# Kernel optimization log

Measured on AMD Instinct MI355X. Metric: run time of the kernel, lower is better.

Reference implementation:

```python
import jax, jax.numpy as jnp
import numpy as np

HID = 128
OUT = 5


def _gru_layer(x, kernel, rkernel, bias):
    # Keras GRU v2 semantics, reset_after=True, activation=tanh, recurrent_activation=sigmoid.
    # x: [B, T, F]; kernel: [F, 3H]; rkernel: [H, 3H]; bias: [2, 3H] (input bias, recurrent bias)
    b_in, b_rec = bias[0], bias[1]
    H = rkernel.shape[0]
    xw = jnp.einsum('btf,fh->bth', x, kernel) + b_in  # precompute input projections [B,T,3H]

    def step(h, xw_t):
        ri = h @ rkernel + b_rec                      # [B, 3H]
        xz, xr, xh = jnp.split(xw_t, 3, axis=-1)
        rz, rr, rh = jnp.split(ri, 3, axis=-1)
        z = jax.nn.sigmoid(xz + rz)
        r = jax.nn.sigmoid(xr + rr)
        hh = jnp.tanh(xh + r * rh)
        h_new = z * h + (1.0 - z) * hh
        return h_new, h_new

    h0 = jnp.zeros((x.shape[0], H), dtype=x.dtype)
    _, hs = jax.lax.scan(step, h0, jnp.swapaxes(xw, 0, 1))  # [T, B, H]
    return jnp.swapaxes(hs, 0, 1)                           # [B, T, H]


def setup_inputs() -> dict:
    key = jax.random.key(0)
    ks = jax.random.split(key, 12)
    B, T, F = 64, 2048, 128
    s = 1.0 / np.sqrt(F)
    inp = {"x": jax.random.normal(ks[0], (B, T, F), dtype=jnp.float32)}
    for i in range(3):
        fin = F if i == 0 else HID
        inp[f"k{i}"] = jax.random.normal(ks[1 + 3 * i], (fin, 3 * HID), dtype=jnp.float32) * s
        inp[f"rk{i}"] = jax.random.normal(ks[2 + 3 * i], (HID, 3 * HID), dtype=jnp.float32) * s
        inp[f"b{i}"] = jnp.zeros((2, 3 * HID), dtype=jnp.float32)
    inp["wo"] = jax.random.normal(ks[10], (HID, OUT), dtype=jnp.float32) * s
    inp["bo"] = jnp.zeros((OUT,), dtype=jnp.float32)
    return inp


def reference(x, k0, rk0, b0, k1, rk1, b1, k2, rk2, b2, wo, bo):
    h = _gru_layer(x, k0, rk0, b0)
    h = _gru_layer(h, k1, rk1, b1)
    h = _gru_layer(h, k2, rk2, b2)
    return h @ wo + bo  # [B, T, OUT]
```

## Files before the change

kernel.cpp:

```cpp
#include <hip/hip_runtime.h>
#include <hip/hip_bf16.h>
#include <hip/hip_fp16.h>


#define HID   128
#define H3    384
#define OUTD  5
#define CHK   16

typedef _Float16 f16x2 __attribute__((ext_vector_type(2)));
typedef _Float16 f16x8 __attribute__((ext_vector_type(8)));

__device__ __forceinline__ float fdot2(f16x2 a, f16x2 b, float c) {
#if __has_builtin(__builtin_amdgcn_fdot2)
    return __builtin_amdgcn_fdot2(a, b, c, false);
#else
    return fmaf((float)a.x, (float)b.x, fmaf((float)a.y, (float)b.y, c));
#endif
}

__device__ __forceinline__ float fexp2(float x) {
#if __has_builtin(__builtin_amdgcn_exp2f)
    return __builtin_amdgcn_exp2f(x);
#else
    return exp2f(x);
#endif
}

__device__ __forceinline__ float frcp(float x) {
#if __has_builtin(__builtin_amdgcn_rcpf)
    return __builtin_amdgcn_rcpf(x);
#else
    return 1.f / x;
#endif
}

__device__ __forceinline__ float fsigmoid(float x) {
    return frcp(1.f + fexp2(x * -1.4426950408889634f));
}

__device__ __forceinline__ float ftanh_(float x) {
    return fmaf(-2.f, frcp(1.f + fexp2(x * 2.8853900817779268f)), 1.f);
}

__device__ __forceinline__ void soft_barrier() {
    asm volatile("s_waitcnt lgkmcnt(0)\n\ts_barrier" ::: "memory");
}

__device__ __forceinline__ float quad_sum(float x) {
#if __has_builtin(__builtin_amdgcn_mov_dpp)
    int i1 = __builtin_amdgcn_mov_dpp(__float_as_int(x), 0xB1, 0xF, 0xF, true);
    x += __int_as_float(i1);
    int i2 = __builtin_amdgcn_mov_dpp(__float_as_int(x), 0x4E, 0xF, 0xF, true);
    x += __int_as_float(i2);
#else
    x += __shfl_xor(x, 1);
    x += __shfl_xor(x, 2);
#endif
    return x;
}

__global__ void zero_flags(int* f) {
    if (threadIdx.x < 192) f[threadIdx.x] = 0;
}

__global__ __launch_bounds__(512, 2) void gru_pipe(
    const float* __restrict__ x,
    const float* __restrict__ k0, const float* __restrict__ k1, const float* __restrict__ k2,
    const float* __restrict__ rk0, const float* __restrict__ rk1, const float* __restrict__ rk2,
    const float* __restrict__ b0, const float* __restrict__ b1, const float* __restrict__ b2,
    _Float16* __restrict__ hpl0, _Float16* __restrict__ hpl1, _Float16* __restrict__ hpl2,
    int* flags, int T)
{
    const int blk   = blockIdx.x;
    const int layer = blk >> 6;
    const int b     = blk & 63;
    const int t     = threadIdx.x;
    const int j     = t >> 2;
    const int kh    = t & 3;
    const int k0i   = kh * 32;
    const int NC    = T / CHK;

    const float* Kw = (layer == 0) ? k0  : (layer == 1) ? k1  : k2;
    const float* Rw = (layer == 0) ? rk0 : (layer == 1) ? rk1 : rk2;
    const float* Bs = (layer == 0) ? b0  : (layer == 1) ? b1  : b2;
    const _Float16* hin = (layer == 1) ? hpl0 : hpl1;
    _Float16* hout = (layer == 0) ? hpl0 : (layer == 1) ? hpl1 : hpl2;

    __shared__ __align__(16) _Float16 hb[2][HID];
    __shared__ __align__(16) _Float16 ins[2][CHK][HID];

    f16x2 wzR[16], wrR[16], whR[16], wzK[16], wrK[16], whK[16];
#pragma unroll
    for (int p = 0; p < 16; ++p) {
        const int k = k0i + 2 * p;
        const float* r0p = Rw + (size_t)k * H3;
        const float* r1p = Rw + (size_t)(k + 1) * H3;
        const float* k0p = Kw + (size_t)k * H3;
        const float* k1p = Kw + (size_t)(k + 1) * H3;
        f16x2 a;
        a.x = (_Float16)r0p[j];       a.y = (_Float16)r1p[j];       wzR[p] = a;
        a.x = (_Float16)r0p[j + 128]; a.y = (_Float16)r1p[j + 128]; wrR[p] = a;
        a.x = (_Float16)r0p[j + 256]; a.y = (_Float16)r1p[j + 256]; whR[p] = a;
        a.x = (_Float16)k0p[j];       a.y = (_Float16)k1p[j];       wzK[p] = a;
        a.x = (_Float16)k0p[j + 128]; a.y = (_Float16)k1p[j + 128]; wrK[p] = a;
        a.x = (_Float16)k0p[j + 256]; a.y = (_Float16)k1p[j + 256]; whK[p] = a;
    }
    const float bzK = Bs[j]       + Bs[384 + j];
    const float brK = Bs[128 + j] + Bs[384 + 128 + j];
    const float bhK = Bs[256 + j];
    const float bhR = Bs[384 + 256 + j];

    int* myflag = flags + layer * 64 + b;
    int* sflag  = flags + (layer - 1) * 64 + b;

    const float*    xb  = x    + (size_t)b * T * HID;
    const _Float16* hib = hin  + (size_t)b * T * HID;
    _Float16*       hob = hout + (size_t)b * T * HID;

    f16x2 sreg[2];
    auto stage_load = [&](int cc) {
#pragma unroll
        for (int i = 0; i < 2; ++i) {
            const int d  = t + 512 * i;
            const int rw = d >> 6;
            const int c2 = d & 63;
            const size_t off = (size_t)(cc * CHK + rw) * HID + 2 * c2;
            if (layer == 0) {
                const float2 v = *(const float2*)(xb + off);
                f16x2 o; o.x = (_Float16)v.x; o.y = (_Float16)v.y;
                sreg[i] = o;
            } else {
                sreg[i] = *(const f16x2*)(hib + off);
            }
        }
    };
    auto stage_write = [&](int cc) {
        const int slot = cc & 1;
#pragma unroll
        for (int i = 0; i < 2; ++i) {
            const int d  = t + 512 * i;
            const int rw = d >> 6;
            const int c2 = d & 63;
            *(f16x2*)(&ins[slot][rw][2 * c2]) = sreg[i];
        }
    };

    if (t < HID) { hb[0][t] = (_Float16)0.f; hb[1][t] = (_Float16)0.f; }

    if (layer > 0 && t == 0) {
        while (__hip_atomic_load(sflag, __ATOMIC_ACQUIRE, __HIP_MEMORY_SCOPE_AGENT) < CHK)
            __builtin_amdgcn_s_sleep(4);
    }
    __syncthreads();
    stage_load(0);
    stage_write(0);
    __syncthreads();

    float xz, xr, xh;
    {
        const f16x8* ip = (const f16x8*)(&ins[0][0][k0i]);
        float pz = 0.f, pr = 0.f, ph = 0.f;
#pragma unroll
        for (int i = 0; i < 4; ++i) {
            union { f16x8 v; f16x2 p[4]; } u;
            u.v = ip[i];
#pragma unroll
            for (int q = 0; q < 4; ++q) {
                pz = fdot2(u.p[q], wzK[4 * i + q], pz);
                pr = fdot2(u.p[q], wrK[4 * i + q], pr);
                ph = fdot2(u.p[q], whK[4 * i + q], ph);
            }
        }
        xz = quad_sum(pz) + bzK;
        xr = quad_sum(pr) + brK;
        xh = quad_sum(ph) + bhK;
    }

    float h_old = 0.f;

    for (int c = 0; c < NC; ++c) {
        __syncthreads();
        if (t == 0) {
            if (layer < 2 && c > 0)
                __hip_atomic_store(myflag, c * CHK, __ATOMIC_RELEASE, __HIP_MEMORY_SCOPE_AGENT);
            if (layer > 0 && c + 1 < NC) {
                while (__hip_atomic_load(sflag, __ATOMIC_ACQUIRE, __HIP_MEMORY_SCOPE_AGENT) < (c + 2) * CHK)
                    __builtin_amdgcn_s_sleep(4);
            }
        }
        __syncthreads();
        if (c + 1 < NC) stage_load(c + 1);

#pragma unroll 2
        for (int ts = 0; ts < CHK; ++ts) {
            const int tstep = c * CHK + ts;
            const int rbuf  = ts & 1;

            const f16x8* hp = (const f16x8*)(&hb[rbuf][k0i]);
            float sz = 0.f, sr = 0.f, sh = 0.f;
#pragma unroll
            for (int i = 0; i < 4; ++i) {
                union { f16x8 v; f16x2 p[4]; } u;
                u.v = hp[i];
#pragma unroll
                for (int q = 0; q < 4; ++q) {
                    sz = fdot2(u.p[q], wzR[4 * i + q], sz);
                    sr = fdot2(u.p[q], wrR[4 * i + q], sr);
                    sh = fdot2(u.p[q], whR[4 * i + q], sh);
                }
            }
            sz = quad_sum(sz); sr = quad_sum(sr); sh = quad_sum(sh);

            const float z  = fsigmoid(xz + sz);
            const float r  = fsigmoid(xr + sr);
            const float hh = ftanh_(xh + (sh + bhR) * r);
            const float hn = fmaf(z, h_old - hh, hh);
            h_old = hn;

            if (kh == 0) {
                hb[rbuf ^ 1][j] = (_Float16)hn;
                hob[(size_t)tstep * HID + j] = (_Float16)hn;
            }

            if (ts == 7 && c + 1 < NC) stage_write(c + 1);

            if (tstep + 1 < T) {
                const int tn = tstep + 1;
                const f16x8* ip = (const f16x8*)(&ins[(tn >> 4) & 1][tn & 15][k0i]);
                float pz = 0.f, pr = 0.f, ph = 0.f;
#pragma unroll
                for (int i = 0; i < 4; ++i) {
                    union { f16x8 v; f16x2 p[4]; } u;
                    u.v = ip[i];
#pragma unroll
                    for (int q = 0; q < 4; ++q) {
                        pz = fdot2(u.p[q], wzK[4 * i + q], pz);
                        pr = fdot2(u.p[q], wrK[4 * i + q], pr);
                        ph = fdot2(u.p[q], whK[4 * i + q], ph);
                    }
                }
                xz = quad_sum(pz) + bzK;
                xr = quad_sum(pr) + brK;
                xh = quad_sum(ph) + bhK;
            }

            soft_barrier();
        }
    }

    __syncthreads();
    if (t == 0 && layer < 2)
        __hip_atomic_store(myflag, T, __ATOMIC_RELEASE, __HIP_MEMORY_SCOPE_AGENT);
}

__global__ __launch_bounds__(256) void out_proj(
    const _Float16* __restrict__ Hf,
    const float* __restrict__ wo,
    const float* __restrict__ bo,
    float*       __restrict__ out,
    int R)
{
    const int r = blockIdx.x * 256 + threadIdx.x;
    if (r >= R) return;
    const f16x8* xp = (const f16x8*)(Hf + (size_t)r * HID);

    float a0 = bo[0], a1 = bo[1], a2 = bo[2], a3 = bo[3], a4 = bo[4];
#pragma unroll 4
    for (int c = 0; c < 16; ++c) {
        const f16x8 v = xp[c];
#pragma unroll
        for (int e = 0; e < 8; ++e) {
            const float xv = (float)v[e];
            const float* w = wo + (size_t)(8 * c + e) * OUTD;
            a0 = fmaf(xv, w[0], a0);
            a1 = fmaf(xv, w[1], a1);
            a2 = fmaf(xv, w[2], a2);
            a3 = fmaf(xv, w[3], a3);
            a4 = fmaf(xv, w[4], a4);
        }
    }
    float* op = out + (size_t)r * OUTD;
    op[0] = a0; op[1] = a1; op[2] = a2; op[3] = a3; op[4] = a4;
}

extern "C" void kernel_launch(void* const* d_in, const int* in_sizes, int n_in,
                              void* d_out, int out_size, void* d_ws, size_t ws_size,
                              hipStream_t stream) {
    const float* x   = (const float*)d_in[0];
    const float* k0  = (const float*)d_in[1];
    const float* rk0 = (const float*)d_in[2];
    const float* b0  = (const float*)d_in[3];
    const float* k1  = (const float*)d_in[4];
    const float* rk1 = (const float*)d_in[5];
    const float* b1  = (const float*)d_in[6];
    const float* k2  = (const float*)d_in[7];
    const float* rk2 = (const float*)d_in[8];
    const float* b2  = (const float*)d_in[9];
    const float* wo  = (const float*)d_in[10];
    const float* bo  = (const float*)d_in[11];
    float* out = (float*)d_out;

    const int BT = in_sizes[0] / HID;
    const int B  = 64;
    const int T  = BT / B;

    const size_t plane = (size_t)BT * HID * sizeof(_Float16);
    _Float16* hpl0 = (_Float16*)d_ws;
    _Float16* hpl1 = (_Float16*)((char*)d_ws + plane);
    _Float16* hpl2 = (_Float16*)((char*)d_ws + 2 * plane);
    int*      flags = (int*)((char*)d_ws + 3 * plane);

    zero_flags<<<1, 256, 0, stream>>>(flags);
    gru_pipe  <<<192, 512, 0, stream>>>(x, k0, k1, k2, rk0, rk1, rk2,
                                        b0, b1, b2, hpl0, hpl1, hpl2, flags, T);
    out_proj  <<<(BT + 255) / 256, 256, 0, stream>>>(hpl2, wo, bo, out, BT);
}
```

Baseline: 1.752 ms.

## Warp-specialize GRU block: dedicated waves compute input projection one step ahead

```diff
diff --git a/kernel.cpp b/kernel.cpp
--- a/kernel.cpp
+++ b/kernel.cpp
@@ -60,11 +60,21 @@
     return x;
 }
 
+__device__ __forceinline__ float pair_sum(float x) {
+#if __has_builtin(__builtin_amdgcn_mov_dpp)
+    int i1 = __builtin_amdgcn_mov_dpp(__float_as_int(x), 0xB1, 0xF, 0xF, true);
+    x += __int_as_float(i1);
+#else
+    x += __shfl_xor(x, 1);
+#endif
+    return x;
+}
+
 __global__ void zero_flags(int* f) {
     if (threadIdx.x < 192) f[threadIdx.x] = 0;
 }
 
-__global__ __launch_bounds__(512, 2) void gru_pipe(
+__global__ __launch_bounds__(768, 3) void gru_pipe(
     const float* __restrict__ x,
     const float* __restrict__ k0, const float* __restrict__ k1, const float* __restrict__ k2,
     const float* __restrict__ rk0, const float* __restrict__ rk1, const float* __restrict__ rk2,
@@ -76,9 +86,6 @@
     const int layer = blk >> 6;
     const int b     = blk & 63;
     const int t     = threadIdx.x;
-    const int j     = t >> 2;
-    const int kh    = t & 3;
-    const int k0i   = kh * 32;
     const int NC    = T / CHK;
 
     const float* Kw = (layer == 0) ? k0  : (layer == 1) ? k1  : k2;
@@ -89,27 +96,7 @@
 
     __shared__ __align__(16) _Float16 hb[2][HID];
     __shared__ __align__(16) _Float16 ins[2][CHK][HID];
-
-    f16x2 wzR[16], wrR[16], whR[16], wzK[16], wrK[16], whK[16];
-#pragma unroll
-    for (int p = 0; p < 16; ++p) {
-        const int k = k0i + 2 * p;
-        const float* r0p = Rw + (size_t)k * H3;
-        const float* r1p = Rw + (size_t)(k + 1) * H3;
-        const float* k0p = Kw + (size_t)k * H3;
-        const float* k1p = Kw + (size_t)(k + 1) * H3;
-        f16x2 a;
-        a.x = (_Float16)r0p[j];       a.y = (_Float16)r1p[j];       wzR[p] = a;
-        a.x = (_Float16)r0p[j + 128]; a.y = (_Float16)r1p[j + 128]; wrR[p] = a;
-        a.x = (_Float16)r0p[j + 256]; a.y = (_Float16)r1p[j + 256]; whR[p] = a;
-        a.x = (_Float16)k0p[j];       a.y = (_Float16)k1p[j];       wzK[p] = a;
-        a.x = (_Float16)k0p[j + 128]; a.y = (_Float16)k1p[j + 128]; wrK[p] = a;
-        a.x = (_Float16)k0p[j + 256]; a.y = (_Float16)k1p[j + 256]; whK[p] = a;
-    }
-    const float bzK = Bs[j]       + Bs[384 + j];
-    const float brK = Bs[128 + j] + Bs[384 + 128 + j];
-    const float bhK = Bs[256 + j];
-    const float bhR = Bs[384 + 256 + j];
+    __shared__ __align__(16) float    xws[2][3][HID];
 
     int* myflag = flags + layer * 64 + b;
     int* sflag  = flags + (layer - 1) * 64 + b;
@@ -118,140 +105,180 @@
     const _Float16* hib = hin  + (size_t)b * T * HID;
     _Float16*       hob = hout + (size_t)b * T * HID;
 
-    f16x2 sreg[2];
-    auto stage_load = [&](int cc) {
-#pragma unroll
-        for (int i = 0; i < 2; ++i) {
-            const int d  = t + 512 * i;
-            const int rw = d >> 6;
-            const int c2 = d & 63;
-            const size_t off = (size_t)(cc * CHK + rw) * HID + 2 * c2;
-            if (layer == 0) {
-                const float2 v = *(const float2*)(xb + off);
-                f16x2 o; o.x = (_Float16)v.x; o.y = (_Float16)v.y;
-                sreg[i] = o;
-            } else {
-                sreg[i] = *(const f16x2*)(hib + off);
-            }
-        }
-    };
-    auto stage_write = [&](int cc) {
-        const int slot = cc & 1;
-#pragma unroll
-        for (int i = 0; i < 2; ++i) {
-            const int d  = t + 512 * i;
-            const int rw = d >> 6;
-            const int c2 = d & 63;
-            *(f16x2*)(&ins[slot][rw][2 * c2]) = sreg[i];
-        }
-    };
-
     if (t < HID) { hb[0][t] = (_Float16)0.f; hb[1][t] = (_Float16)0.f; }
 
-    if (layer > 0 && t == 0) {
-        while (__hip_atomic_load(sflag, __ATOMIC_ACQUIRE, __HIP_MEMORY_SCOPE_AGENT) < CHK)
-            __builtin_amdgcn_s_sleep(4);
-    }
-    __syncthreads();
-    stage_load(0);
-    stage_write(0);
-    __syncthreads();
-
-    float xz, xr, xh;
-    {
-        const f16x8* ip = (const f16x8*)(&ins[0][0][k0i]);
-        float pz = 0.f, pr = 0.f, ph = 0.f;
-#pragma unroll
-        for (int i = 0; i < 4; ++i) {
-            union { f16x8 v; f16x2 p[4]; } u;
-            u.v = ip[i];
-#pragma unroll
-            for (int q = 0; q < 4; ++q) {
-                pz = fdot2(u.p[q], wzK[4 * i + q], pz);
-                pr = fdot2(u.p[q], wrK[4 * i + q], pr);
-                ph = fdot2(u.p[q], whK[4 * i + q], ph);
-            }
-        }
-        xz = quad_sum(pz) + bzK;
-        xr = quad_sum(pr) + brK;
-        xh = quad_sum(ph) + bhK;
-    }
-
-    float h_old = 0.f;
-
-    for (int c = 0; c < NC; ++c) {
-        __syncthreads();
-        if (t == 0) {
-            if (layer < 2 && c > 0)
-                __hip_atomic_store(myflag, c * CHK, __ATOMIC_RELEASE, __HIP_MEMORY_SCOPE_AGENT);
-            if (layer > 0 && c + 1 < NC) {
-                while (__hip_atomic_load(sflag, __ATOMIC_ACQUIRE, __HIP_MEMORY_SCOPE_AGENT) < (c + 2) * CHK)
-                    __builtin_amdgcn_s_sleep(4);
-            }
-        }
-        __syncthreads();
-        if (c + 1 < NC) stage_load(c + 1);
+    if (t < 512) {
+        __builtin_amdgcn_s_setprio(1);
+        const int j   = t >> 2;
+        const int kh  = t & 3;
+        const int k0i = kh * 32;
+
+        f16x2 wzR[16], wrR[16], whR[16];
+#pragma unroll
+        for (int p = 0; p < 16; ++p) {
+            const int k = k0i + 2 * p;
+            const float* r0p = Rw + (size_t)k * H3;
+            const float* r1p = r0p + H3;
+            f16x2 a;
+            a.x = (_Float16)r0p[j];       a.y = (_Float16)r1p[j];       wzR[p] = a;
+            a.x = (_Float16)r0p[j + 128]; a.y = (_Float16)r1p[j + 128]; wrR[p] = a;
+            a.x = (_Float16)r0p[j + 256]; a.y = (_Float16)r1p[j + 256]; whR[p] = a;
+        }
+        const float bhR = Bs[H3 + 256 + j];
+
+        if (layer > 0 && t == 0) {
+            while (__hip_atomic_load(sflag, __ATOMIC_ACQUIRE, __HIP_MEMORY_SCOPE_AGENT) < CHK)
+                __builtin_amdgcn_s_sleep(4);
+        }
+        __syncthreads();
+        __syncthreads();
+        __syncthreads();
+
+        float h_old = 0.f;
+        for (int c = 0; c < NC; ++c) {
+            __syncthreads();
+            if (t == 0) {
+                if (layer < 2 && c > 0)
+                    __hip_atomic_store(myflag, c * CHK, __ATOMIC_RELEASE, __HIP_MEMORY_SCOPE_AGENT);
+                if (layer > 0 && c + 1 < NC) {
+                    while (__hip_atomic_load(sflag, __ATOMIC_ACQUIRE, __HIP_MEMORY_SCOPE_AGENT) < (c + 2) * CHK)
+                        __builtin_amdgcn_s_sleep(4);
+                }
+            }
+            __syncthreads();
 
 #pragma unroll 2
-        for (int ts = 0; ts < CHK; ++ts) {
-            const int tstep = c * CHK + ts;
-            const int rbuf  = ts & 1;
-
-            const f16x8* hp = (const f16x8*)(&hb[rbuf][k0i]);
-            float sz = 0.f, sr = 0.f, sh = 0.f;
-#pragma unroll
-            for (int i = 0; i < 4; ++i) {
-                union { f16x8 v; f16x2 p[4]; } u;
-                u.v = hp[i];
-#pragma unroll
-                for (int q = 0; q < 4; ++q) {
-                    sz = fdot2(u.p[q], wzR[4 * i + q], sz);
-                    sr = fdot2(u.p[q], wrR[4 * i + q], sr);
-                    sh = fdot2(u.p[q], whR[4 * i + q], sh);
-                }
-            }
-            sz = quad_sum(sz); sr = quad_sum(sr); sh = quad_sum(sh);
-
-            const float z  = fsigmoid(xz + sz);
-            const float r  = fsigmoid(xr + sr);
-            const float hh = ftanh_(xh + (sh + bhR) * r);
-            const float hn = fmaf(z, h_old - hh, hh);
-            h_old = hn;
-
-            if (kh == 0) {
-                hb[rbuf ^ 1][j] = (_Float16)hn;
-                hob[(size_t)tstep * HID + j] = (_Float16)hn;
-            }
-
-            if (ts == 7 && c + 1 < NC) stage_write(c + 1);
-
-            if (tstep + 1 < T) {
-                const int tn = tstep + 1;
-                const f16x8* ip = (const f16x8*)(&ins[(tn >> 4) & 1][tn & 15][k0i]);
-                float pz = 0.f, pr = 0.f, ph = 0.f;
+            for (int ts = 0; ts < CHK; ++ts) {
+                const int tstep = c * CHK + ts;
+                const int rbuf  = ts & 1;
+
+                const float* xwp = &xws[rbuf][0][j];
+                const float xz = xwp[0], xr = xwp[HID], xh = xwp[2 * HID];
+
+                const f16x8* hp = (const f16x8*)(&hb[rbuf][k0i]);
+                float sz = 0.f, sr = 0.f, sh = 0.f;
 #pragma unroll
                 for (int i = 0; i < 4; ++i) {
                     union { f16x8 v; f16x2 p[4]; } u;
-                    u.v = ip[i];
+                    u.v = hp[i];
 #pragma unroll
                     for (int q = 0; q < 4; ++q) {
-                        pz = fdot2(u.p[q], wzK[4 * i + q], pz);
-                        pr = fdot2(u.p[q], wrK[4 * i + q], pr);
-                        ph = fdot2(u.p[q], whK[4 * i + q], ph);
+                        sz = fdot2(u.p[q], wzR[4 * i + q], sz);
+                        sr = fdot2(u.p[q], wrR[4 * i + q], sr);
+                        sh = fdot2(u.p[q], whR[4 * i + q], sh);
                     }
                 }
-                xz = quad_sum(pz) + bzK;
-                xr = quad_sum(pr) + brK;
-                xh = quad_sum(ph) + bhK;
-            }
-
-            soft_barrier();
-        }
+                sz = quad_sum(sz); sr = quad_sum(sr); sh = quad_sum(sh);
+
+                const float z  = fsigmoid(xz + sz);
+                const float r  = fsigmoid(xr + sr);
+                const float hh = ftanh_(xh + (sh + bhR) * r);
+                const float hn = fmaf(z, h_old - hh, hh);
+                h_old = hn;
+
+                if (kh == 0) {
+                    hb[rbuf ^ 1][j] = (_Float16)hn;
+                    hob[(size_t)tstep * HID + j] = (_Float16)hn;
+                }
+                soft_barrier();
+            }
+        }
+        __syncthreads();
+        if (t == 0 && layer < 2)
+            __hip_atomic_store(myflag, T, __ATOMIC_RELEASE, __HIP_MEMORY_SCOPE_AGENT);
+
+    } else {
+        const int p  = t - 512;
+        const int o  = p >> 1;
+        const int kp = p & 1;
+
+        f16x2 wzK[32], wrK[32], whK[32];
+#pragma unroll
+        for (int i = 0; i < 32; ++i) {
+            const int k = kp * 64 + 2 * i;
+            const float* c0 = Kw + (size_t)k * H3;
+            const float* c1 = c0 + H3;
+            f16x2 a;
+            a.x = (_Float16)c0[o];       a.y = (_Float16)c1[o];       wzK[i] = a;
+            a.x = (_Float16)c0[o + 128]; a.y = (_Float16)c1[o + 128]; wrK[i] = a;
+            a.x = (_Float16)c0[o + 256]; a.y = (_Float16)c1[o + 256]; whK[i] = a;
+        }
+        const float bz = Bs[o]       + Bs[H3 + o];
+        const float br = Bs[128 + o] + Bs[H3 + 128 + o];
+        const float bh = Bs[256 + o];
+
+        f16x2 sreg[4];
+        auto stage_load = [&](int cc) {
+#pragma unroll
+            for (int i = 0; i < 4; ++i) {
+                const int d  = p + 256 * i;
+                const int rw = d >> 6;
+                const int c2 = d & 63;
+                const size_t off = (size_t)(cc * CHK + rw) * HID + 2 * c2;
+                if (layer == 0) {
+                    const float2 v = *(const float2*)(xb + off);
+                    f16x2 oo; oo.x = (_Float16)v.x; oo.y = (_Float16)v.y;
+                    sreg[i] = oo;
+                } else {
+                    sreg[i] = *(const f16x2*)(hib + off);
+                }
+            }
+        };
+        auto stage_write = [&](int cc) {
+            const int slot = cc & 1;
+#pragma unroll
+            for (int i = 0; i < 4; ++i) {
+                const int d  = p + 256 * i;
+                const int rw = d >> 6;
+                const int c2 = d & 63;
+                *(f16x2*)(&ins[slot][rw][2 * c2]) = sreg[i];
+            }
+        };
+        auto proj_step = [&](int tn) {
+            const f16x8* ip = (const f16x8*)(&ins[(tn >> 4) & 1][tn & 15][kp * 64]);
+            float pz = 0.f, pr = 0.f, ph = 0.f;
+#pragma unroll
+            for (int i = 0; i < 8; ++i) {
+                union { f16x8 v; f16x2 q[4]; } u;
+                u.v = ip[i];
+#pragma unroll
+                for (int q2 = 0; q2 < 4; ++q2) {
+                    pz = fdot2(u.q[q2], wzK[4 * i + q2], pz);
+                    pr = fdot2(u.q[q2], wrK[4 * i + q2], pr);
+                    ph = fdot2(u.q[q2], whK[4 * i + q2], ph);
+                }
+            }
+            pz = pair_sum(pz); pr = pair_sum(pr); ph = pair_sum(ph);
+            if (kp == 0) {
+                float* xo = &xws[tn & 1][0][o];
+                xo[0]       = pz + bz;
+                xo[HID]     = pr + br;
+                xo[2 * HID] = ph + bh;
+            }
+        };
+
+        __syncthreads();
+        stage_load(0);
+        stage_write(0);
+        __syncthreads();
+        proj_step(0);
+        __syncthreads();
+
+        for (int c = 0; c < NC; ++c) {
+            __syncthreads();
+            __syncthreads();
+            if (c + 1 < NC) stage_load(c + 1);
+
+#pragma unroll 2
+            for (int ts = 0; ts < CHK; ++ts) {
+                const int tn = c * CHK + ts + 1;
+                if (tn < T) proj_step(tn);
+                if (ts == 7 && c + 1 < NC) stage_write(c + 1);
+                soft_barrier();
+            }
+        }
+        __syncthreads();
     }
-
-    __syncthreads();
-    if (t == 0 && layer < 2)
-        __hip_atomic_store(myflag, T, __ATOMIC_RELEASE, __HIP_MEMORY_SCOPE_AGENT);
 }
 
 __global__ __launch_bounds__(256) void out_proj(
@@ -312,7 +339,7 @@
     int*      flags = (int*)((char*)d_ws + 3 * plane);
 
     zero_flags<<<1, 256, 0, stream>>>(flags);
-    gru_pipe  <<<192, 512, 0, stream>>>(x, k0, k1, k2, rk0, rk1, rk2,
+    gru_pipe  <<<192, 768, 0, stream>>>(x, k0, k1, k2, rk0, rk1, rk2,
                                         b0, b1, b2, hpl0, hpl1, hpl2, flags, T);
     out_proj  <<<(BT + 255) / 256, 256, 0, stream>>>(hpl2, wo, bo, out, BT);
 }
```

Measured after the change: 2.039 ms. 16.4% more time.

## Process two batch rows per GRU block to reuse register-resident weights

Applied to the files above, without the earlier changes.

```diff
diff --git a/kernel.cpp b/kernel.cpp
--- a/kernel.cpp
+++ b/kernel.cpp
@@ -61,7 +61,7 @@
 }
 
 __global__ void zero_flags(int* f) {
-    if (threadIdx.x < 192) f[threadIdx.x] = 0;
+    if (threadIdx.x < 96) f[threadIdx.x] = 0;
 }
 
 __global__ __launch_bounds__(512, 2) void gru_pipe(
@@ -73,8 +73,10 @@
     int* flags, int T)
 {
     const int blk   = blockIdx.x;
-    const int layer = blk >> 6;
-    const int b     = blk & 63;
+    const int layer = blk >> 5;
+    const int pair  = blk & 31;
+    const int bA    = pair * 2;
+    const int bB    = bA + 1;
     const int t     = threadIdx.x;
     const int j     = t >> 2;
     const int kh    = t & 3;
@@ -87,17 +89,17 @@
     const _Float16* hin = (layer == 1) ? hpl0 : hpl1;
     _Float16* hout = (layer == 0) ? hpl0 : (layer == 1) ? hpl1 : hpl2;
 
-    __shared__ __align__(16) _Float16 hb[2][HID];
-    __shared__ __align__(16) _Float16 ins[2][CHK][HID];
+    __shared__ __align__(16) _Float16 hb[2][2][HID];
+    __shared__ __align__(16) _Float16 ins[2][2][CHK][HID];
 
     f16x2 wzR[16], wrR[16], whR[16], wzK[16], wrK[16], whK[16];
 #pragma unroll
     for (int p = 0; p < 16; ++p) {
         const int k = k0i + 2 * p;
         const float* r0p = Rw + (size_t)k * H3;
-        const float* r1p = Rw + (size_t)(k + 1) * H3;
+        const float* r1p = r0p + H3;
         const float* k0p = Kw + (size_t)k * H3;
-        const float* k1p = Kw + (size_t)(k + 1) * H3;
+        const float* k1p = k0p + H3;
         f16x2 a;
         a.x = (_Float16)r0p[j];       a.y = (_Float16)r1p[j];       wzR[p] = a;
         a.x = (_Float16)r0p[j + 128]; a.y = (_Float16)r1p[j + 128]; wrR[p] = a;
@@ -106,19 +108,22 @@
         a.x = (_Float16)k0p[j + 128]; a.y = (_Float16)k1p[j + 128]; wrK[p] = a;
         a.x = (_Float16)k0p[j + 256]; a.y = (_Float16)k1p[j + 256]; whK[p] = a;
     }
-    const float bzK = Bs[j]       + Bs[384 + j];
-    const float brK = Bs[128 + j] + Bs[384 + 128 + j];
+    const float bzK = Bs[j]       + Bs[H3 + j];
+    const float brK = Bs[128 + j] + Bs[H3 + 128 + j];
     const float bhK = Bs[256 + j];
-    const float bhR = Bs[384 + 256 + j];
-
-    int* myflag = flags + layer * 64 + b;
-    int* sflag  = flags + (layer - 1) * 64 + b;
-
-    const float*    xb  = x    + (size_t)b * T * HID;
-    const _Float16* hib = hin  + (size_t)b * T * HID;
-    _Float16*       hob = hout + (size_t)b * T * HID;
-
-    f16x2 sreg[2];
+    const float bhR = Bs[H3 + 256 + j];
+
+    int* myflag = flags + layer * 32 + pair;
+    int* sflag  = flags + (layer - 1) * 32 + pair;
+
+    const float*    xbA  = x    + (size_t)bA * T * HID;
+    const float*    xbB  = x    + (size_t)bB * T * HID;
+    const _Float16* hibA = hin  + (size_t)bA * T * HID;
+    const _Float16* hibB = hin  + (size_t)bB * T * HID;
+    _Float16*       hobA = hout + (size_t)bA * T * HID;
+    _Float16*       hobB = hout + (size_t)bB * T * HID;
+
+    f16x2 sregA[2], sregB[2];
     auto stage_load = [&](int cc) {
 #pragma unroll
         for (int i = 0; i < 2; ++i) {
@@ -127,11 +132,14 @@
             const int c2 = d & 63;
             const size_t off = (size_t)(cc * CHK + rw) * HID + 2 * c2;
             if (layer == 0) {
-                const float2 v = *(const float2*)(xb + off);
-                f16x2 o; o.x = (_Float16)v.x; o.y = (_Float16)v.y;
-                sreg[i] = o;
+                const float2 vA = *(const float2*)(xbA + off);
+                const float2 vB = *(const float2*)(xbB + off);
+                f16x2 oA; oA.x = (_Float16)vA.x; oA.y = (_Float16)vA.y;
+                f16x2 oB; oB.x = (_Float16)vB.x; oB.y = (_Float16)vB.y;
+                sregA[i] = oA; sregB[i] = oB;
             } else {
-                sreg[i] = *(const f16x2*)(hib + off);
+                sregA[i] = *(const f16x2*)(hibA + off);
+                sregB[i] = *(const f16x2*)(hibB + off);
             }
         }
     };
@@ -142,11 +150,33 @@
             const int d  = t + 512 * i;
             const int rw = d >> 6;
             const int c2 = d & 63;
-            *(f16x2*)(&ins[slot][rw][2 * c2]) = sreg[i];
+            *(f16x2*)(&ins[slot][0][rw][2 * c2]) = sregA[i];
+            *(f16x2*)(&ins[slot][1][rw][2 * c2]) = sregB[i];
         }
     };
-
-    if (t < HID) { hb[0][t] = (_Float16)0.f; hb[1][t] = (_Float16)0.f; }
+    auto proj_one = [&](int tn, int bat, float& oz, float& orr, float& oh) {
+        const f16x8* ip = (const f16x8*)(&ins[(tn >> 4) & 1][bat][tn & 15][k0i]);
+        float pz = 0.f, pr = 0.f, ph = 0.f;
+#pragma unroll
+        for (int i = 0; i < 4; ++i) {
+            union { f16x8 v; f16x2 p[4]; } u;
+            u.v = ip[i];
+#pragma unroll
+            for (int q = 0; q < 4; ++q) {
+                pz = fdot2(u.p[q], wzK[4 * i + q], pz);
+                pr = fdot2(u.p[q], wrK[4 * i + q], pr);
+                ph = fdot2(u.p[q], whK[4 * i + q], ph);
+            }
+        }
+        oz = quad_sum(pz) + bzK;
+        orr = quad_sum(pr) + brK;
+        oh = quad_sum(ph) + bhK;
+    };
+
+    if (t < HID) {
+        hb[0][0][t] = (_Float16)0.f; hb[0][1][t] = (_Float16)0.f;
+        hb[1][0][t] = (_Float16)0.f; hb[1][1][t] = (_Float16)0.f;
+    }
 
     if (layer > 0 && t == 0) {
         while (__hip_atomic_load(sflag, __ATOMIC_ACQUIRE, __HIP_MEMORY_SCOPE_AGENT) < CHK)
@@ -157,27 +187,11 @@
     stage_write(0);
     __syncthreads();
 
-    float xz, xr, xh;
-    {
-        const f16x8* ip = (const f16x8*)(&ins[0][0][k0i]);
-        float pz = 0.f, pr = 0.f, ph = 0.f;
-#pragma unroll
-        for (int i = 0; i < 4; ++i) {
-            union { f16x8 v; f16x2 p[4]; } u;
-            u.v = ip[i];
-#pragma unroll
-            for (int q = 0; q < 4; ++q) {
-                pz = fdot2(u.p[q], wzK[4 * i + q], pz);
-                pr = fdot2(u.p[q], wrK[4 * i + q], pr);
-                ph = fdot2(u.p[q], whK[4 * i + q], ph);
-            }
-        }
-        xz = quad_sum(pz) + bzK;
-        xr = quad_sum(pr) + brK;
-        xh = quad_sum(ph) + bhK;
-    }
-
-    float h_old = 0.f;
+    float xzA, xrA, xhA, xzB, xrB, xhB;
+    proj_one(0, 0, xzA, xrA, xhA);
+    proj_one(0, 1, xzB, xrB, xhB);
+
+    float hoA = 0.f, hoB = 0.f;
 
     for (int c = 0; c < NC; ++c) {
         __syncthreads();
@@ -197,52 +211,51 @@
             const int tstep = c * CHK + ts;
             const int rbuf  = ts & 1;
 
-            const f16x8* hp = (const f16x8*)(&hb[rbuf][k0i]);
-            float sz = 0.f, sr = 0.f, sh = 0.f;
+            const f16x8* hpA = (const f16x8*)(&hb[0][rbuf][k0i]);
+            const f16x8* hpB = (const f16x8*)(&hb[1][rbuf][k0i]);
+            float szA = 0.f, srA = 0.f, shA = 0.f;
+            float szB = 0.f, srB = 0.f, shB = 0.f;
 #pragma unroll
             for (int i = 0; i < 4; ++i) {
-                union { f16x8 v; f16x2 p[4]; } u;
-                u.v = hp[i];
+                union { f16x8 v; f16x2 p[4]; } uA, uB;
+                uA.v = hpA[i];
+                uB.v = hpB[i];
 #pragma unroll
                 for (int q = 0; q < 4; ++q) {
-                    sz = fdot2(u.p[q], wzR[4 * i + q], sz);
-                    sr = fdot2(u.p[q], wrR[4 * i + q], sr);
-                    sh = fdot2(u.p[q], whR[4 * i + q], sh);
+                    szA = fdot2(uA.p[q], wzR[4 * i + q], szA);
+                    szB = fdot2(uB.p[q], wzR[4 * i + q], szB);
+                    srA = fdot2(uA.p[q], wrR[4 * i + q], srA);
+                    srB = fdot2(uB.p[q], wrR[4 * i + q], srB);
+                    shA = fdot2(uA.p[q], whR[4 * i + q], shA);
+                    shB = fdot2(uB.p[q], whR[4 * i + q], shB);
                 }
             }
-            sz = quad_sum(sz); sr = quad_sum(sr); sh = quad_sum(sh);
-
-            const float z  = fsigmoid(xz + sz);
-            const float r  = fsigmoid(xr + sr);
-            const float hh = ftanh_(xh + (sh + bhR) * r);
-            const float hn = fmaf(z, h_old - hh, hh);
-            h_old = hn;
+            szA = quad_sum(szA); szB = quad_sum(szB);
+            srA = quad_sum(srA); srB = quad_sum(srB);
+            shA = quad_sum(shA); shB = quad_sum(shB);
+
+            const float zA  = fsigmoid(xzA + szA);
+            const float zB  = fsigmoid(xzB + szB);
+            const float rA  = fsigmoid(xrA + srA);
+            const float rB  = fsigmoid(xrB + srB);
+            const float hhA = ftanh_(xhA + (shA + bhR) * rA);
+            const float hhB = ftanh_(xhB + (shB + bhR) * rB);
+            const float hnA = fmaf(zA, hoA - hhA, hhA);
+            const float hnB = fmaf(zB, hoB - hhB, hhB);
+            hoA = hnA; hoB = hnB;
 
             if (kh == 0) {
-                hb[rbuf ^ 1][j] = (_Float16)hn;
-                hob[(size_t)tstep * HID + j] = (_Float16)hn;
+                hb[0][rbuf ^ 1][j] = (_Float16)hnA;
+                hb[1][rbuf ^ 1][j] = (_Float16)hnB;
+                hobA[(size_t)tstep * HID + j] = (_Float16)hnA;
+                hobB[(size_t)tstep * HID + j] = (_Float16)hnB;
             }
 
             if (ts == 7 && c + 1 < NC) stage_write(c + 1);
 
             if (tstep + 1 < T) {
-                const int tn = tstep + 1;
-                const f16x8* ip = (const f16x8*)(&ins[(tn >> 4) & 1][tn & 15][k0i]);
-                float pz = 0.f, pr = 0.f, ph = 0.f;
-#pragma unroll
-                for (int i = 0; i < 4; ++i) {
-                    union { f16x8 v; f16x2 p[4]; } u;
-                    u.v = ip[i];
-#pragma unroll
-                    for (int q = 0; q < 4; ++q) {
-                        pz = fdot2(u.p[q], wzK[4 * i + q], pz);
-                        pr = fdot2(u.p[q], wrK[4 * i + q], pr);
-                        ph = fdot2(u.p[q], whK[4 * i + q], ph);
-                    }
-                }
-                xz = quad_sum(pz) + bzK;
-                xr = quad_sum(pr) + brK;
-                xh = quad_sum(ph) + bhK;
+                proj_one(tstep + 1, 0, xzA, xrA, xhA);
+                proj_one(tstep + 1, 1, xzB, xrB, xhB);
             }
 
             soft_barrier();
@@ -311,8 +324,8 @@
     _Float16* hpl2 = (_Float16*)((char*)d_ws + 2 * plane);
     int*      flags = (int*)((char*)d_ws + 3 * plane);
 
-    zero_flags<<<1, 256, 0, stream>>>(flags);
-    gru_pipe  <<<192, 512, 0, stream>>>(x, k0, k1, k2, rk0, rk1, rk2,
-                                        b0, b1, b2, hpl0, hpl1, hpl2, flags, T);
+    zero_flags<<<1, 96, 0, stream>>>(flags);
+    gru_pipe  <<<96, 512, 0, stream>>>(x, k0, k1, k2, rk0, rk1, rk2,
+                                       b0, b1, b2, hpl0, hpl1, hpl2, flags, T);
     out_proj  <<<(BT + 255) / 256, 256, 0, stream>>>(hpl2, wo, bo, out, BT);
 }
```

New measurement: 2.941 ms. 67.9% more time.

## Offload input projections to producer blocks feeding recurrent blocks via ring buffers

Applied to the files above, without the earlier changes.

```diff
diff --git a/kernel.cpp b/kernel.cpp
--- a/kernel.cpp
+++ b/kernel.cpp
@@ -7,8 +7,11 @@
 #define H3    384
 #define OUTD  5
 #define CHK   16
+#define RING  4
+#define NREC  192
 
 typedef _Float16 f16x2 __attribute__((ext_vector_type(2)));
+typedef _Float16 f16x4 __attribute__((ext_vector_type(4)));
 typedef _Float16 f16x8 __attribute__((ext_vector_type(8)));
 
 __device__ __forceinline__ float fdot2(f16x2 a, f16x2 b, float c) {
@@ -61,7 +64,7 @@
 }
 
 __global__ void zero_flags(int* f) {
-    if (threadIdx.x < 192) f[threadIdx.x] = 0;
+    if (threadIdx.x < 384) f[threadIdx.x] = 0;
 }
 
 __global__ __launch_bounds__(512, 2) void gru_pipe(
@@ -70,188 +73,254 @@
     const float* __restrict__ rk0, const float* __restrict__ rk1, const float* __restrict__ rk2,
     const float* __restrict__ b0, const float* __restrict__ b1, const float* __restrict__ b2,
     _Float16* __restrict__ hpl0, _Float16* __restrict__ hpl1, _Float16* __restrict__ hpl2,
+    float* __restrict__ xwr,
     int* flags, int T)
 {
-    const int blk   = blockIdx.x;
-    const int layer = blk >> 6;
-    const int b     = blk & 63;
-    const int t     = threadIdx.x;
-    const int j     = t >> 2;
-    const int kh    = t & 3;
-    const int k0i   = kh * 32;
-    const int NC    = T / CHK;
-
-    const float* Kw = (layer == 0) ? k0  : (layer == 1) ? k1  : k2;
-    const float* Rw = (layer == 0) ? rk0 : (layer == 1) ? rk1 : rk2;
-    const float* Bs = (layer == 0) ? b0  : (layer == 1) ? b1  : b2;
-    const _Float16* hin = (layer == 1) ? hpl0 : hpl1;
-    _Float16* hout = (layer == 0) ? hpl0 : (layer == 1) ? hpl1 : hpl2;
+    const int blk = blockIdx.x;
+    const int t   = threadIdx.x;
+    const int NC  = T / CHK;
 
     __shared__ __align__(16) _Float16 hb[2][HID];
-    __shared__ __align__(16) _Float16 ins[2][CHK][HID];
-
-    f16x2 wzR[16], wrR[16], whR[16], wzK[16], wrK[16], whK[16];
-#pragma unroll
-    for (int p = 0; p < 16; ++p) {
-        const int k = k0i + 2 * p;
-        const float* r0p = Rw + (size_t)k * H3;
-        const float* r1p = Rw + (size_t)(k + 1) * H3;
-        const float* k0p = Kw + (size_t)k * H3;
-        const float* k1p = Kw + (size_t)(k + 1) * H3;
-        f16x2 a;
-        a.x = (_Float16)r0p[j];       a.y = (_Float16)r1p[j];       wzR[p] = a;
-        a.x = (_Float16)r0p[j + 128]; a.y = (_Float16)r1p[j + 128]; wrR[p] = a;
-        a.x = (_Float16)r0p[j + 256]; a.y = (_Float16)r1p[j + 256]; whR[p] = a;
-        a.x = (_Float16)k0p[j];       a.y = (_Float16)k1p[j];       wzK[p] = a;
-        a.x = (_Float16)k0p[j + 128]; a.y = (_Float16)k1p[j + 128]; wrK[p] = a;
-        a.x = (_Float16)k0p[j + 256]; a.y = (_Float16)k1p[j + 256]; whK[p] = a;
-    }
-    const float bzK = Bs[j]       + Bs[384 + j];
-    const float brK = Bs[128 + j] + Bs[384 + 128 + j];
-    const float bhK = Bs[256 + j];
-    const float bhR = Bs[384 + 256 + j];
-
-    int* myflag = flags + layer * 64 + b;
-    int* sflag  = flags + (layer - 1) * 64 + b;
-
-    const float*    xb  = x    + (size_t)b * T * HID;
-    const _Float16* hib = hin  + (size_t)b * T * HID;
-    _Float16*       hob = hout + (size_t)b * T * HID;
-
-    f16x2 sreg[2];
-    auto stage_load = [&](int cc) {
-#pragma unroll
-        for (int i = 0; i < 2; ++i) {
-            const int d  = t + 512 * i;
-            const int rw = d >> 6;
-            const int c2 = d & 63;
-            const size_t off = (size_t)(cc * CHK + rw) * HID + 2 * c2;
-            if (layer == 0) {
-                const float2 v = *(const float2*)(xb + off);
-                f16x2 o; o.x = (_Float16)v.x; o.y = (_Float16)v.y;
-                sreg[i] = o;
-            } else {
-                sreg[i] = *(const f16x2*)(hib + off);
-            }
-        }
-    };
-    auto stage_write = [&](int cc) {
-        const int slot = cc & 1;
-#pragma unroll
-        for (int i = 0; i < 2; ++i) {
-            const int d  = t + 512 * i;
-            const int rw = d >> 6;
-            const int c2 = d & 63;
-            *(f16x2*)(&ins[slot][rw][2 * c2]) = sreg[i];
-        }
-    };
-
-    if (t < HID) { hb[0][t] = (_Float16)0.f; hb[1][t] = (_Float16)0.f; }
-
-    if (layer > 0 && t == 0) {
-        while (__hip_atomic_load(sflag, __ATOMIC_ACQUIRE, __HIP_MEMORY_SCOPE_AGENT) < CHK)
-            __builtin_amdgcn_s_sleep(4);
-    }
-    __syncthreads();
-    stage_load(0);
-    stage_write(0);
-    __syncthreads();
-
-    float xz, xr, xh;
-    {
-        const f16x8* ip = (const f16x8*)(&ins[0][0][k0i]);
-        float pz = 0.f, pr = 0.f, ph = 0.f;
-#pragma unroll
-        for (int i = 0; i < 4; ++i) {
-            union { f16x8 v; f16x2 p[4]; } u;
-            u.v = ip[i];
-#pragma unroll
-            for (int q = 0; q < 4; ++q) {
-                pz = fdot2(u.p[q], wzK[4 * i + q], pz);
-                pr = fdot2(u.p[q], wrK[4 * i + q], pr);
-                ph = fdot2(u.p[q], whK[4 * i + q], ph);
-            }
-        }
-        xz = quad_sum(pz) + bzK;
-        xr = quad_sum(pr) + brK;
-        xh = quad_sum(ph) + bhK;
-    }
-
-    float h_old = 0.f;
-
-    for (int c = 0; c < NC; ++c) {
+    __shared__ __align__(16) float    xwc[2][CHK][H3];
+    __shared__ __align__(16) _Float16 ins_p[CHK][HID];
+
+    if (blk < NREC) {
+        const int layer = blk >> 6;
+        const int b     = blk & 63;
+        const int j     = t >> 2;
+        const int kh    = t & 3;
+        const int k0i   = kh * 32;
+
+        const float* Rw = (layer == 0) ? rk0 : (layer == 1) ? rk1 : rk2;
+        const float* Bs = (layer == 0) ? b0  : (layer == 1) ? b1  : b2;
+        _Float16* hout = (layer == 0) ? hpl0 : (layer == 1) ? hpl1 : hpl2;
+
+        f16x2 wzR[16], wrR[16], whR[16];
+#pragma unroll
+        for (int p = 0; p < 16; ++p) {
+            const int k = k0i + 2 * p;
+            const float* r0p = Rw + (size_t)k * H3;
+            const float* r1p = r0p + H3;
+            f16x2 a;
+            a.x = (_Float16)r0p[j];       a.y = (_Float16)r1p[j];       wzR[p] = a;
+            a.x = (_Float16)r0p[j + 128]; a.y = (_Float16)r1p[j + 128]; wrR[p] = a;
+            a.x = (_Float16)r0p[j + 256]; a.y = (_Float16)r1p[j + 256]; whR[p] = a;
+        }
+        const float bhR = Bs[H3 + 256 + j];
+
+        int* hflag = flags + layer * 64 + b;
+        int* pflag = flags + NREC + layer * 64 + b;
+
+        _Float16* hob = hout + (size_t)b * T * HID;
+        const float* ringb = xwr + (size_t)(layer * 64 + b) * RING * CHK * H3;
+
+        float4 sreg[3];
+        auto stage_load = [&](int cc) {
+            const float* base = ringb + (size_t)(cc & (RING - 1)) * CHK * H3;
+#pragma unroll
+            for (int i = 0; i < 3; ++i) {
+                const int f = t + 512 * i;
+                sreg[i] = *(const float4*)(base + 4 * f);
+            }
+        };
+        auto stage_write = [&](int cc) {
+            float* dst = &xwc[cc & 1][0][0];
+#pragma unroll
+            for (int i = 0; i < 3; ++i) {
+                const int f = t + 512 * i;
+                *(float4*)(dst + 4 * f) = sreg[i];
+            }
+        };
+
+        if (t < HID) { hb[0][t] = (_Float16)0.f; hb[1][t] = (_Float16)0.f; }
+
+        if (t == 0) {
+            while (__hip_atomic_load(pflag, __ATOMIC_ACQUIRE, __HIP_MEMORY_SCOPE_AGENT) < CHK)
+                __builtin_amdgcn_s_sleep(4);
+        }
         __syncthreads();
-        if (t == 0) {
-            if (layer < 2 && c > 0)
-                __hip_atomic_store(myflag, c * CHK, __ATOMIC_RELEASE, __HIP_MEMORY_SCOPE_AGENT);
-            if (layer > 0 && c + 1 < NC) {
-                while (__hip_atomic_load(sflag, __ATOMIC_ACQUIRE, __HIP_MEMORY_SCOPE_AGENT) < (c + 2) * CHK)
-                    __builtin_amdgcn_s_sleep(4);
-            }
-        }
+        stage_load(0);
+        stage_write(0);
         __syncthreads();
-        if (c + 1 < NC) stage_load(c + 1);
-
+        if (t == 0)
+            __hip_atomic_store(hflag, 1, __ATOMIC_RELEASE, __HIP_MEMORY_SCOPE_AGENT);
+
+        float h_old = 0.f;
+        for (int c = 0; c < NC; ++c) {
+            __syncthreads();
+            if (t == 0) {
+                if (c > 0)
+                    __hip_atomic_store(hflag, c * CHK, __ATOMIC_RELEASE, __HIP_MEMORY_SCOPE_AGENT);
+                if (c + 1 < NC) {
+                    while (__hip_atomic_load(pflag, __ATOMIC_ACQUIRE, __HIP_MEMORY_SCOPE_AGENT) < (c + 2) * CHK)
+                        __builtin_amdgcn_s_sleep(4);
+                }
+            }
+            __syncthreads();
+            if (c + 1 < NC) stage_load(c + 1);
+
+            const float* xrow = &xwc[c & 1][0][0];
 #pragma unroll 2
-        for (int ts = 0; ts < CHK; ++ts) {
-            const int tstep = c * CHK + ts;
-            const int rbuf  = ts & 1;
-
-            const f16x8* hp = (const f16x8*)(&hb[rbuf][k0i]);
-            float sz = 0.f, sr = 0.f, sh = 0.f;
-#pragma unroll
-            for (int i = 0; i < 4; ++i) {
-                union { f16x8 v; f16x2 p[4]; } u;
-                u.v = hp[i];
-#pragma unroll
-                for (int q = 0; q < 4; ++q) {
-                    sz = fdot2(u.p[q], wzR[4 * i + q], sz);
-                    sr = fdot2(u.p[q], wrR[4 * i + q], sr);
-                    sh = fdot2(u.p[q], whR[4 * i + q], sh);
-                }
-            }
-            sz = quad_sum(sz); sr = quad_sum(sr); sh = quad_sum(sh);
-
-            const float z  = fsigmoid(xz + sz);
-            const float r  = fsigmoid(xr + sr);
-            const float hh = ftanh_(xh + (sh + bhR) * r);
-            const float hn = fmaf(z, h_old - hh, hh);
-            h_old = hn;
-
-            if (kh == 0) {
-                hb[rbuf ^ 1][j] = (_Float16)hn;
-                hob[(size_t)tstep * HID + j] = (_Float16)hn;
-            }
-
-            if (ts == 7 && c + 1 < NC) stage_write(c + 1);
-
-            if (tstep + 1 < T) {
-                const int tn = tstep + 1;
-                const f16x8* ip = (const f16x8*)(&ins[(tn >> 4) & 1][tn & 15][k0i]);
-                float pz = 0.f, pr = 0.f, ph = 0.f;
+            for (int ts = 0; ts < CHK; ++ts) {
+                const int tstep = c * CHK + ts;
+                const int rbuf  = ts & 1;
+
+                const float xz = xrow[ts * H3 + j];
+                const float xr = xrow[ts * H3 + 128 + j];
+                const float xh = xrow[ts * H3 + 256 + j];
+
+                const f16x8* hp = (const f16x8*)(&hb[rbuf][k0i]);
+                float sz = 0.f, sr = 0.f, sh = 0.f;
 #pragma unroll
                 for (int i = 0; i < 4; ++i) {
                     union { f16x8 v; f16x2 p[4]; } u;
-                    u.v = ip[i];
+                    u.v = hp[i];
 #pragma unroll
                     for (int q = 0; q < 4; ++q) {
-                        pz = fdot2(u.p[q], wzK[4 * i + q], pz);
-                        pr = fdot2(u.p[q], wrK[4 * i + q], pr);
-                        ph = fdot2(u.p[q], whK[4 * i + q], ph);
+                        sz = fdot2(u.p[q], wzR[4 * i + q], sz);
+                        sr = fdot2(u.p[q], wrR[4 * i + q], sr);
+                        sh = fdot2(u.p[q], whR[4 * i + q], sh);
                     }
                 }
-                xz = quad_sum(pz) + bzK;
-                xr = quad_sum(pr) + brK;
-                xh = quad_sum(ph) + bhK;
-            }
-
-            soft_barrier();
+                sz = quad_sum(sz); sr = quad_sum(sr); sh = quad_sum(sh);
+
+                const float z  = fsigmoid(xz + sz);
+                const float r  = fsigmoid(xr + sr);
+                const float hh = ftanh_(xh + (sh + bhR) * r);
+                const float hn = fmaf(z, h_old - hh, hh);
+                h_old = hn;
+
+                if (kh == 0) {
+                    hb[rbuf ^ 1][j] = (_Float16)hn;
+                    hob[(size_t)tstep * HID + j] = (_Float16)hn;
+                }
+
+                if (ts == 7 && c + 1 < NC) stage_write(c + 1);
+
+                soft_barrier();
+            }
+        }
+
+        __syncthreads();
+        if (t == 0)
+            __hip_atomic_store(hflag, T, __ATOMIC_RELEASE, __HIP_MEMORY_SCOPE_AGENT);
+
+    } else {
+        const int b   = blk - NREC;
+        const int j   = t >> 2;
+        const int kh  = t & 3;
+        const int k0i = kh * 32;
+
+        f16x2 wK[3][3][16];
+        float bzc[3], brc[3], bhc[3];
+#pragma unroll
+        for (int l = 0; l < 3; ++l) {
+            const float* Kl = (l == 0) ? k0 : (l == 1) ? k1 : k2;
+            const float* Bl = (l == 0) ? b0 : (l == 1) ? b1 : b2;
+#pragma unroll
+            for (int p = 0; p < 16; ++p) {
+                const int k = k0i + 2 * p;
+                const float* c0 = Kl + (size_t)k * H3;
+                const float* c1 = c0 + H3;
+                f16x2 a;
+                a.x = (_Float16)c0[j];       a.y = (_Float16)c1[j];       wK[l][0][p] = a;
+                a.x = (_Float16)c0[j + 128]; a.y = (_Float16)c1[j + 128]; wK[l][1][p] = a;
+                a.x = (_Float16)c0[j + 256]; a.y = (_Float16)c1[j + 256]; wK[l][2][p] = a;
+            }
+            bzc[l] = Bl[j]       + Bl[H3 + j];
+            brc[l] = Bl[128 + j] + Bl[H3 + 128 + j];
+            bhc[l] = Bl[256 + j];
+        }
+
+        int* hf[3] = { flags + b, flags + 64 + b, flags + 128 + b };
+        int* pf[3] = { flags + NREC + b, flags + NREC + 64 + b, flags + NREC + 128 + b };
+
+        const float*    xbp = x    + (size_t)b * T * HID;
+        const _Float16* h0b = hpl0 + (size_t)b * T * HID;
+        const _Float16* h1b = hpl1 + (size_t)b * T * HID;
+
+        const int row  = t >> 5;
+        const int col4 = (t & 31) * 4;
+
+        auto wait_ge = [&](int* f, int v) {
+            if (t == 0) {
+                while (__hip_atomic_load(f, __ATOMIC_ACQUIRE, __HIP_MEMORY_SCOPE_AGENT) < v)
+                    __builtin_amdgcn_s_sleep(4);
+            }
+            __syncthreads();
+        };
+
+        auto do_chunk = [&](int l, int cc) {
+            if (l == 0) {
+                const float4 v = *(const float4*)(xbp + (size_t)(cc * CHK + row) * HID + col4);
+                f16x4 o;
+                o[0] = (_Float16)v.x; o[1] = (_Float16)v.y;
+                o[2] = (_Float16)v.z; o[3] = (_Float16)v.w;
+                *(f16x4*)(&ins_p[row][col4]) = o;
+            } else {
+                const _Float16* hs = (l == 1) ? h0b : h1b;
+                *(f16x4*)(&ins_p[row][col4]) =
+                    *(const f16x4*)(hs + (size_t)(cc * CHK + row) * HID + col4);
+            }
+            __syncthreads();
+
+            float* ring = xwr + ((size_t)(l * 64 + b) * RING + (cc & (RING - 1))) * CHK * H3;
+            const float bz = bzc[l], br = brc[l], bh = bhc[l];
+
+#pragma unroll 2
+            for (int rp = 0; rp < 8; ++rp) {
+                const int r0 = 2 * rp, r1 = r0 + 1;
+                const f16x8* p0 = (const f16x8*)(&ins_p[r0][k0i]);
+                const f16x8* p1 = (const f16x8*)(&ins_p[r1][k0i]);
+                float az0 = 0.f, ar0 = 0.f, ah0 = 0.f;
+                float az1 = 0.f, ar1 = 0.f, ah1 = 0.f;
+#pragma unroll
+                for (int i = 0; i < 4; ++i) {
+                    union { f16x8 v; f16x2 p[4]; } u0, u1;
+                    u0.v = p0[i]; u1.v = p1[i];
+#pragma unroll
+                    for (int q = 0; q < 4; ++q) {
+                        az0 = fdot2(u0.p[q], wK[l][0][4 * i + q], az0);
+                        az1 = fdot2(u1.p[q], wK[l][0][4 * i + q], az1);
+                        ar0 = fdot2(u0.p[q], wK[l][1][4 * i + q], ar0);
+                        ar1 = fdot2(u1.p[q], wK[l][1][4 * i + q], ar1);
+                        ah0 = fdot2(u0.p[q], wK[l][2][4 * i + q], ah0);
+                        ah1 = fdot2(u1.p[q], wK[l][2][4 * i + q], ah1);
+                    }
+                }
+                az0 = quad_sum(az0); ar0 = quad_sum(ar0); ah0 = quad_sum(ah0);
+                az1 = quad_sum(az1); ar1 = quad_sum(ar1); ah1 = quad_sum(ah1);
+                if (kh == 0) {
+                    float* o0 = ring + (size_t)r0 * H3;
+                    o0[j] = az0 + bz; o0[128 + j] = ar0 + br; o0[256 + j] = ah0 + bh;
+                    float* o1 = ring + (size_t)r1 * H3;
+                    o1[j] = az1 + bz; o1[128 + j] = ar1 + br; o1[256 + j] = ah1 + bh;
+                }
+            }
+            __syncthreads();
+            if (t == 0)
+                __hip_atomic_store(pf[l], (cc + 1) * CHK, __ATOMIC_RELEASE, __HIP_MEMORY_SCOPE_AGENT);
+        };
+
+        for (int i = 0; i < NC + 4; ++i) {
+            if (i < NC) {
+                if (i >= RING) wait_ge(hf[0], (i == RING) ? 1 : (i - RING) * CHK);
+                do_chunk(0, i);
+            }
+            if (i >= 2 && i - 2 < NC) {
+                const int cc = i - 2;
+                wait_ge(hf[0], (cc + 1) * CHK);
+                if (cc >= RING) wait_ge(hf[1], (cc == RING) ? 1 : (cc - RING) * CHK);
+                do_chunk(1, cc);
+            }
+            if (i >= 4 && i - 4 < NC) {
+                const int cc = i - 4;
+                wait_ge(hf[1], (cc + 1) * CHK);
+                if (cc >= RING) wait_ge(hf[2], (cc == RING) ? 1 : (cc - RING) * CHK);
+                do_chunk(2, cc);
+            }
         }
     }
-
-    __syncthreads();
-    if (t == 0 && layer < 2)
-        __hip_atomic_store(myflag, T, __ATOMIC_RELEASE, __HIP_MEMORY_SCOPE_AGENT);
 }
 
 __global__ __launch_bounds__(256) void out_proj(
@@ -306,13 +375,15 @@
     const int T  = BT / B;
 
     const size_t plane = (size_t)BT * HID * sizeof(_Float16);
+    const size_t ringb = (size_t)3 * 64 * RING * CHK * H3 * sizeof(float);
     _Float16* hpl0 = (_Float16*)d_ws;
     _Float16* hpl1 = (_Float16*)((char*)d_ws + plane);
     _Float16* hpl2 = (_Float16*)((char*)d_ws + 2 * plane);
-    int*      flags = (int*)((char*)d_ws + 3 * plane);
-
-    zero_flags<<<1, 256, 0, stream>>>(flags);
-    gru_pipe  <<<192, 512, 0, stream>>>(x, k0, k1, k2, rk0, rk1, rk2,
-                                        b0, b1, b2, hpl0, hpl1, hpl2, flags, T);
+    float*    xwr  = (float*)((char*)d_ws + 3 * plane);
+    int*      flags = (int*)((char*)d_ws + 3 * plane + ringb);
+
+    zero_flags<<<1, 512, 0, stream>>>(flags);
+    gru_pipe  <<<256, 512, 0, stream>>>(x, k0, k1, k2, rk0, rk1, rk2,
+                                        b0, b1, b2, hpl0, hpl1, hpl2, xwr, flags, T);
     out_proj  <<<(BT + 255) / 256, 256, 0, stream>>>(hpl2, wo, bo, out, BT);
 }
```

New measurement: 4.306 ms. 146% more time.
